# Optimization experiments

Hardware: AMD Instinct MI355X
Metric: run time of the kernel (lower is better)

## Reference

```python
import jax, jax.numpy as jnp
import numpy as np

A, H, HI = 4, 3, 2  # nagents, n_pol_heads, n_intr_rew_heads (sep_extr_head=True)
# leave-one-out index table: row i lists all agents k != i, in ascending order (torch loop order)
LOO = np.array([[k for k in range(A) if k != i] for i in range(A)])  # [A, A-1]


def setup_inputs() -> dict:
    key = jax.random.key(0)
    ks = jax.random.split(key, 12)
    B, S, C, D = 32768, 256, 16, 128  # batch, vect_state_size, action_size, hidden_dim
    IN = C * (A - 1) + D  # 176 critic input dim
    r = lambda k, shp, s=0.05: jax.random.normal(k, shp, dtype=jnp.float32) * s
    return {
        "state_vect": jax.random.normal(ks[0], (B, S), dtype=jnp.float32),
        "acs": jax.random.normal(ks[1], (A, H, B, C), dtype=jnp.float32),
        "enc_W": r(ks[2], (S, D)),
        "enc_b": r(ks[3], (D,)),
        "extr_W1": r(ks[4], (H, A, IN, D)),
        "extr_b1": r(ks[5], (H, A, D)),
        "extr_W2": r(ks[6], (H, A, D, C)),
        "extr_b2": r(ks[7], (H, A, C)),
        "intr_W1": r(ks[8], (HI, A, IN, D)),
        "intr_b1": r(ks[9], (HI, A, D)),
        "intr_W2": r(ks[10], (HI, A, D, C)),
        "intr_b2": r(ks[11], (HI, A, C)),
    }


def reference(state_vect, acs, enc_W, enc_b, extr_W1, extr_b1, extr_W2, extr_b2,
              intr_W1, intr_b1, intr_W2, intr_b2):
    B, C = acs.shape[2], acs.shape[3]
    D = enc_W.shape[1]
    # shared state encoder: Linear -> ReLU
    enc = jax.nn.relu(state_vect @ enc_W + enc_b)  # [B, D]
    # leave-one-out action concat per (agent, head): cat(acs[k!=i, j]) ++ enc
    rel = acs[LOO]                                 # [A, A-1, H, B, C]
    rel = rel.transpose(0, 2, 3, 1, 4).reshape(A, H, B, (A - 1) * C)
    x = jnp.concatenate([rel, jnp.broadcast_to(enc, (A, H, B, D))], axis=-1)  # [A,H,B,IN]
    # greedy action index of agent i's own head-j policy output
    int_acs = jnp.argmax(acs, axis=-1)             # [A, H, B]

    def critic(xin, W1, b1, W2, b2):
        # xin: [A, Hc, B, IN]; W1: [Hc, A, IN, D]; W2: [Hc, A, D, C]
        h = jax.nn.relu(jnp.einsum('ahbi,haid->ahbd', xin, W1)
                        + b1.transpose(1, 0, 2)[:, :, None, :])
        return (jnp.einsum('ahbd,hadc->ahbc', h, W2)
                + b2.transpose(1, 0, 2)[:, :, None, :])  # [A, Hc, B, C]

    extr_all_q = critic(x, extr_W1, extr_b1, extr_W2, extr_b2)          # [A,H,B,C]
    extr_q = jnp.take_along_axis(extr_all_q, int_acs[..., None], axis=-1)  # [A,H,B,1]
    # intr critics exist only for heads j>=1 (sep_extr_head=True -> offset -1)
    intr_all_q = critic(x[:, 1:], intr_W1, intr_b1, intr_W2, intr_b2)   # [A,HI,B,C]
    intr_q = jnp.take_along_axis(intr_all_q, int_acs[:, 1:, :, None], axis=-1)  # [A,HI,B,1]
    return extr_q, intr_q
```

## Files before the change

### kernel.cpp

```cpp
#include <hip/hip_runtime.h>

#define NA 4
#define NH 3
#define NHI 2
#define Bsz 32768
#define Ssz 256
#define Csz 16
#define Dsz 128
#define INsz 176
#define NP 20
#define KP 192
#define GT 2

typedef __bf16 v8bf __attribute__((ext_vector_type(8)));
typedef float v4f __attribute__((ext_vector_type(4)));

#define OFF_ENC    0
#define OFF_ACSBF  8388608
#define OFF_W1F    20971520
#define OFF_ENCWF  21954560
#define OFF_W2T    22020096
#define OFF_AMX    22102016
#define OFF_ZERO   22495232

#define N_ACSROW (NA*NH*Bsz)
#define N_W1F   (NP*192*32)
#define N_ENCWF (256*32)
#define N_W2T   (NP*Csz*Dsz)
#define N_ZERO  16
#define N_PREP  (N_ACSROW+N_W1F+N_ENCWF+N_W2T+N_ZERO)

__global__ __launch_bounds__(256) void prep_kernel(
    const float* __restrict__ acs, const float* __restrict__ encW,
    const float* __restrict__ eW1, const float* __restrict__ iW1,
    const float* __restrict__ eW2, const float* __restrict__ iW2,
    const float* __restrict__ eb1, const float* __restrict__ ib1,
    char* __restrict__ ws)
{
    long tid = (long)blockIdx.x * 256 + threadIdx.x;

    if (tid < N_ACSROW) {
        const float4* src = (const float4*)(acs + (size_t)tid * 16);
        float4 f0 = src[0], f1 = src[1], f2 = src[2], f3 = src[3];
        float v[16] = {f0.x,f0.y,f0.z,f0.w, f1.x,f1.y,f1.z,f1.w,
                       f2.x,f2.y,f2.z,f2.w, f3.x,f3.y,f3.z,f3.w};
        v8bf o0, o1;
        #pragma unroll
        for (int i = 0; i < 8; ++i) { o0[i] = (__bf16)v[i]; o1[i] = (__bf16)v[8 + i]; }
        v8bf* dst = (v8bf*)(ws + OFF_ACSBF) + tid * 2;
        dst[0] = o0; dst[1] = o1;
        float best = v[0]; int bi = 0;
        #pragma unroll
        for (int c = 1; c < 16; ++c) if (v[c] > best) { best = v[c]; bi = c; }
        ((unsigned char*)(ws + OFF_AMX))[tid] = (unsigned char)bi;
        return;
    }
    tid -= N_ACSROW;
    if (tid < N_W1F) {
        const int n4 = (int)(tid & 31) * 4;
        const int k  = (int)((tid >> 5) % 192);
        const int p  = (int)(tid / 6144);
        const float* W1; const float* B1;
        if (p < 12) { int ai = p / 3, hj = p % 3; int wi = hj * NA + ai;
                      W1 = eW1 + (size_t)wi * INsz * Dsz; B1 = eb1 + (size_t)wi * Dsz; }
        else { int qq = p - 12; int ai = qq >> 1, jj = qq & 1; int wi = jj * NA + ai;
               W1 = iW1 + (size_t)wi * INsz * Dsz; B1 = ib1 + (size_t)wi * Dsz; }
        float4 f;
        if (k < INsz)       f = *(const float4*)(W1 + (size_t)k * Dsz + n4);
        else if (k == INsz) f = *(const float4*)(B1 + n4);
        else                f = (float4){0.f, 0.f, 0.f, 0.f};
        const int kc = k >> 5, q = (k >> 3) & 3, j = k & 7;
        __bf16* dst = (__bf16*)(ws + OFF_W1F);
        const float fv[4] = {f.x, f.y, f.z, f.w};
        #pragma unroll
        for (int i = 0; i < 4; ++i) {
            const int n = n4 + i, nt = n >> 4, m = n & 15;
            dst[((size_t)(p * 6 + kc) * 8 + nt) * 512 + (q * 16 + m) * 8 + j] = (__bf16)fv[i];
        }
        return;
    }
    tid -= N_W1F;
    if (tid < N_ENCWF) {
        const int n4 = (int)(tid & 31) * 4;
        const int k  = (int)(tid >> 5);
        float4 f = *(const float4*)(encW + (size_t)k * Dsz + n4);
        const int kc = k >> 5, q = (k >> 3) & 3, j = k & 7;
        __bf16* dst = (__bf16*)(ws + OFF_ENCWF);
        const float fv[4] = {f.x, f.y, f.z, f.w};
        #pragma unroll
        for (int i = 0; i < 4; ++i) {
            const int n = n4 + i, nt = n >> 4, m = n & 15;
            dst[((size_t)kc * 8 + nt) * 512 + (q * 16 + m) * 8 + j] = (__bf16)fv[i];
        }
        return;
    }
    tid -= N_ENCWF;
    if (tid < N_W2T) {
        int d = (int)(tid & 127);
        int rest = (int)(tid >> 7);
        int c = rest & 15, p = rest >> 4;
        const float* W2;
        if (p < 12) { int ai = p / 3, hj = p % 3; W2 = eW2 + (size_t)(hj * NA + ai) * Dsz * Csz; }
        else { int qq = p - 12; int ai = qq >> 1, jj = qq & 1; W2 = iW2 + (size_t)(jj * NA + ai) * Dsz * Csz; }
        const int dlow = d & 15, dt = d >> 4;
        ((__bf16*)(ws + OFF_W2T))[(size_t)p * 2048 + c * 128 + ((dlow ^ c) * 8) + dt]
            = (__bf16)W2[(size_t)d * Csz + c];
        return;
    }
    tid -= N_W2T;
    if (tid < N_ZERO) {
        ((unsigned int*)(ws + OFF_ZERO))[tid] = (tid == 0) ? 0x00003F80u : 0u;
    }
}

__global__ __launch_bounds__(256) void enc_kernel(const float* __restrict__ sv,
                                                  const float* __restrict__ encb,
                                                  char* __restrict__ ws)
{
    __shared__ __bf16 tb[4][16 * 136];

    const int t = threadIdx.x;
    const int wv = t >> 6, lane = t & 63, m = lane & 15, q = lane >> 4;
    const int R = blockIdx.x * 64 + wv * 16 + m;
    const __bf16* encwf = (const __bf16*)(ws + OFF_ENCWF);
    char* enct = ws + OFF_ENC;

    v4f acc[8];
    #pragma unroll
    for (int nt = 0; nt < 8; ++nt) acc[nt] = (v4f){0.f, 0.f, 0.f, 0.f};

    const float* arow = sv + (size_t)R * Ssz + q * 8;
    #pragma unroll
    for (int kc = 0; kc < 8; ++kc) {
        float4 f0 = *(const float4*)(arow + kc * 32);
        float4 f1 = *(const float4*)(arow + kc * 32 + 4);
        v8bf af;
        af[0]=(__bf16)f0.x; af[1]=(__bf16)f0.y; af[2]=(__bf16)f0.z; af[3]=(__bf16)f0.w;
        af[4]=(__bf16)f1.x; af[5]=(__bf16)f1.y; af[6]=(__bf16)f1.z; af[7]=(__bf16)f1.w;
        #pragma unroll
        for (int nt = 0; nt < 8; ++nt) {
            v8bf bf = *(const v8bf*)(encwf + ((size_t)kc * 8 + nt) * 512 + lane * 8);
            acc[nt] = __builtin_amdgcn_mfma_f32_16x16x32_bf16(af, bf, acc[nt], 0, 0, 0);
        }
    }
    #pragma unroll
    for (int nt = 0; nt < 8; ++nt) {
        const float bias = encb[nt * 16 + m];
        #pragma unroll
        for (int rg = 0; rg < 4; ++rg) {
            float v = acc[nt][rg] + bias;
            v = v > 0.f ? v : 0.f;
            tb[wv][(q * 4 + rg) * 136 + nt * 16 + m] = (__bf16)v;
        }
    }
    __syncthreads();
    const int rt = blockIdx.x * 4 + wv;
    #pragma unroll
    for (int kc = 0; kc < 4; ++kc) {
        v8bf v = *(const v8bf*)&tb[wv][m * 136 + kc * 32 + q * 8];
        *(v8bf*)(enct + ((size_t)(rt * 4 + kc) * 64 + lane) * 16) = v;
    }
}

#define LD_AF(D, KC, GG) \
  { _Pragma("unroll") \
    for (int mt_ = 0; mt_ < 4; ++mt_) \
      D[mt_] = *(const v8bf*)(base[KC] + (size_t)((mt_ + 16 * (GG)) * strd[KC])); }

#define MFMA_KC(AF, KC) \
  { _Pragma("unroll") \
    for (int nt_ = 0; nt_ < 8; ++nt_) { \
      v8bf bf_ = *(const v8bf*)&w1s[(size_t)(((KC) * 8 + nt_) * 512) + lane * 8]; \
      acc[0][nt_] = __builtin_amdgcn_mfma_f32_16x16x32_bf16(bf_, AF[0], acc[0][nt_], 0, 0, 0); \
      acc[1][nt_] = __builtin_amdgcn_mfma_f32_16x16x32_bf16(bf_, AF[1], acc[1][nt_], 0, 0, 0); \
      acc[2][nt_] = __builtin_amdgcn_mfma_f32_16x16x32_bf16(bf_, AF[2], acc[2][nt_], 0, 0, 0); \
      acc[3][nt_] = __builtin_amdgcn_mfma_f32_16x16x32_bf16(bf_, AF[3], acc[3][nt_], 0, 0, 0); \
    } }

__global__ __launch_bounds__(256, 2) void critic_kernel(
    const float* __restrict__ eb2, const float* __restrict__ ib2,
    const char* __restrict__ ws, float* __restrict__ out)
{
    __shared__ __bf16 w1s[6 * 8 * 512];
    __shared__ __bf16 w2s[16 * 128];

    const int t = threadIdx.x;
    const int p  = blockIdx.y;
    const int rb = blockIdx.x;
    const int wv = t >> 6, lane = t & 63, m = lane & 15, q = lane >> 4;

    int ai, hj;
    const float* b2;
    float* outp;
    if (p < 12) {
        ai = p / 3; hj = p % 3;
        b2 = eb2 + (size_t)(hj * NA + ai) * Csz;
        outp = out + (size_t)(ai * NH + hj) * Bsz;
    } else {
        const int qq = p - 12; ai = qq >> 1; const int jj = qq & 1; hj = jj + 1;
        b2 = ib2 + (size_t)(jj * NA + ai) * Csz;
        outp = out + (size_t)NA * NH * Bsz + (size_t)(ai * NHI + jj) * Bsz;
    }

    const char* acsb = ws + OFF_ACSBF;
    const char* enct = ws + OFF_ENC;
    const __bf16* w1f = (const __bf16*)(ws + OFF_W1F) + (size_t)p * 6 * 8 * 512;
    const __bf16* w2t = (const __bf16*)(ws + OFF_W2T) + (size_t)p * 2048;
    const unsigned char* amxp = (const unsigned char*)(ws + OFF_AMX)
        + (size_t)(ai * NH + hj) * Bsz + (size_t)rb * 512 + wv * 64;
    const char* zerop = ws + OFF_ZERO;

    {
        const v8bf* src = (const v8bf*)w1f;
        #pragma unroll
        for (int i = 0; i < 12; ++i)
            ((v8bf*)w1s)[i * 256 + t] = src[i * 256 + t];
        ((v8bf*)w2s)[t] = ((const v8bf*)w2t)[t];
    }

    const int loo0 = 0 + (0 >= ai), loo1 = 1 + (1 >= ai), loo2 = 2 + (2 >= ai);
    const size_t rowoff = ((size_t)rb * 512 + wv * 64 + m) * 32;
    const char* pl0 = acsb + (size_t)(loo0 * NH + hj) * Bsz * 32 + rowoff;
    const char* pl1 = acsb + (size_t)(loo1 * NH + hj) * Bsz * 32 + rowoff;
    const char* pl2 = acsb + (size_t)(loo2 * NH + hj) * Bsz * 32 + rowoff;
    const int rt0 = rb * 32 + wv * 4;
    const char* encB = enct + (size_t)rt0 * 4096 + m * 16;

    const char* base[6];
    int strd[6];
    base[0] = (q < 2) ? (pl0 + q * 16) : (pl1 + (q - 2) * 16);           strd[0] = 512;
    base[1] = (q < 2) ? (pl2 + q * 16) : (encB + (q - 2) * 256);         strd[1] = (q < 2) ? 512 : 4096;
    base[2] = encB + (q + 2)  * 256;                                     strd[2] = 4096;
    base[3] = encB + (q + 6)  * 256;                                     strd[3] = 4096;
    base[4] = encB + (q + 10) * 256;                                     strd[4] = 4096;
    base[5] = (q < 2) ? (encB + (14 + q) * 256) : (zerop + (q - 2) * 16);
    strd[5] = (q < 2) ? 4096 : 0;

    v4f acc[4][8];
    #pragma unroll
    for (int i = 0; i < 4; ++i)
        #pragma unroll
        for (int j = 0; j < 8; ++j)
            acc[i][j] = (v4f){0.f, 0.f, 0.f, 0.f};

    v8bf af0[4], af1[4], af2[4];
    LD_AF(af0, 0, 0)
    LD_AF(af1, 1, 0)

    __syncthreads();

    #pragma unroll
    for (int g = 0; g < GT; ++g) {
        int cb[4];
        #pragma unroll
        for (int mt = 0; mt < 4; ++mt)
            cb[mt] = amxp[g * 256 + mt * 16 + m];

        LD_AF(af2, 2, g)  MFMA_KC(af0, 0)
        LD_AF(af0, 3, g)  MFMA_KC(af1, 1)
        LD_AF(af1, 4, g)  MFMA_KC(af2, 2)
        LD_AF(af2, 5, g)  MFMA_KC(af0, 3)
        if (g + 1 < GT) { LD_AF(af0, 0, g + 1) }
        MFMA_KC(af1, 4)
        if (g + 1 < GT) { LD_AF(af1, 1, g + 1) }
        MFMA_KC(af2, 5)

        #pragma unroll
        for (int mt = 0; mt < 4; ++mt) {
            const int c = cb[mt];
            const __bf16* wcb = &w2s[c * 128];
            float s0 = 0.f, s1 = 0.f;
            #pragma unroll
            for (int rg = 0; rg < 4; rg += 2) {
                const v8bf wa = *(const v8bf*)&wcb[((q * 4 + rg) ^ c) * 8];
                const v8bf wb = *(const v8bf*)&wcb[((q * 4 + rg + 1) ^ c) * 8];
                #pragma unroll
                for (int nt = 0; nt < 8; ++nt) {
                    s0 += fmaxf(acc[mt][nt][rg],     0.f) * (float)wa[nt];
                    s1 += fmaxf(acc[mt][nt][rg + 1], 0.f) * (float)wb[nt];
                }
            }
            float tsum = s0 + s1;
            tsum += __shfl_xor(tsum, 16, 64);
            tsum += __shfl_xor(tsum, 32, 64);
            if (q == 0)
                outp[(size_t)rb * 512 + g * 256 + wv * 64 + mt * 16 + m] = tsum + b2[c];
            if (g + 1 < GT) {
                #pragma unroll
                for (int nt = 0; nt < 8; ++nt) acc[mt][nt] = (v4f){0.f, 0.f, 0.f, 0.f};
            }
        }
    }
}

extern "C" void kernel_launch(void* const* d_in, const int* in_sizes, int n_in,
                              void* d_out, int out_size, void* d_ws, size_t ws_size,
                              hipStream_t stream) {
    const float* sv   = (const float*)d_in[0];
    const float* acs  = (const float*)d_in[1];
    const float* encW = (const float*)d_in[2];
    const float* encb = (const float*)d_in[3];
    const float* eW1  = (const float*)d_in[4];
    const float* eb1  = (const float*)d_in[5];
    const float* eW2  = (const float*)d_in[6];
    const float* eb2  = (const float*)d_in[7];
    const float* iW1  = (const float*)d_in[8];
    const float* ib1  = (const float*)d_in[9];
    const float* iW2  = (const float*)d_in[10];
    const float* ib2  = (const float*)d_in[11];
    float* out = (float*)d_out;
    char* ws = (char*)d_ws;

    hipLaunchKernelGGL(prep_kernel, dim3((N_PREP + 255) / 256), dim3(256), 0, stream,
                       acs, encW, eW1, iW1, eW2, iW2, eb1, ib1, ws);
    hipLaunchKernelGGL(enc_kernel, dim3(Bsz / 64), dim3(256), 0, stream, sv, encb, ws);
    hipLaunchKernelGGL(critic_kernel, dim3(Bsz / 512, NP), dim3(256), 0, stream,
                       eb2, ib2, ws, out);
}
```

Before: 162.0 us.

## Reorder K dimension and tile acs bf16 layout for contiguous MFMA fragment loads

Permutes the critic input K ordering so the encoder features come first and the leave-one-out actions last, and rewrites the bf16 action buffer into a row-tile fragment layout. Each wave's A-fragment loads then become contiguous 1KB-per-wave reads with fixed offsets instead of per-lane base/stride tables. It also moves the amax index load after the MFMAs and caches b2 in shared memory. The risk is that the new layouts must match exactly between the prep kernel and the critic kernel.

New measurement: 153.1 us. 1.06x faster.

```diff
diff --git a/kernel.cpp b/kernel.cpp
--- a/kernel.cpp
+++ b/kernel.cpp
@@ -47,8 +47,12 @@
         v8bf o0, o1;
         #pragma unroll
         for (int i = 0; i < 8; ++i) { o0[i] = (__bf16)v[i]; o1[i] = (__bf16)v[8 + i]; }
-        v8bf* dst = (v8bf*)(ws + OFF_ACSBF) + tid * 2;
-        dst[0] = o0; dst[1] = o1;
+        const int plane = (int)(tid >> 15);
+        const int b     = (int)(tid & 32767);
+        const int rt    = b >> 4, mm = b & 15;
+        char* dstb = ws + OFF_ACSBF + (size_t)plane * 1048576 + (size_t)rt * 512 + mm * 16;
+        *(v8bf*)dstb         = o0;
+        *(v8bf*)(dstb + 256) = o1;
         float best = v[0]; int bi = 0;
         #pragma unroll
         for (int c = 1; c < 16; ++c) if (v[c] > best) { best = v[c]; bi = c; }
@@ -66,7 +70,8 @@
         else { int qq = p - 12; int ai = qq >> 1, jj = qq & 1; int wi = jj * NA + ai;
                W1 = iW1 + (size_t)wi * INsz * Dsz; B1 = ib1 + (size_t)wi * Dsz; }
         float4 f;
-        if (k < INsz)       f = *(const float4*)(W1 + (size_t)k * Dsz + n4);
+        if (k < 128)        f = *(const float4*)(W1 + (size_t)(48 + k) * Dsz + n4);
+        else if (k < INsz)  f = *(const float4*)(W1 + (size_t)(k - 128) * Dsz + n4);
         else if (k == INsz) f = *(const float4*)(B1 + n4);
         else                f = (float4){0.f, 0.f, 0.f, 0.f};
         const int kc = k >> 5, q = (k >> 3) & 3, j = k & 7;
@@ -162,10 +167,20 @@
     }
 }
 
-#define LD_AF(D, KC, GG) \
+#define LD_E(D, KC, GG) \
   { _Pragma("unroll") \
     for (int mt_ = 0; mt_ < 4; ++mt_) \
-      D[mt_] = *(const v8bf*)(base[KC] + (size_t)((mt_ + 16 * (GG)) * strd[KC])); }
+      D[mt_] = *(const v8bf*)(encL + (GG) * 65536 + mt_ * 4096 + (KC) * 1024); }
+
+#define LD_4(D, GG) \
+  { _Pragma("unroll") \
+    for (int mt_ = 0; mt_ < 4; ++mt_) \
+      D[mt_] = *(const v8bf*)(a4L + (GG) * 8192 + mt_ * 512); }
+
+#define LD_5(D, GG) \
+  { _Pragma("unroll") \
+    for (int mt_ = 0; mt_ < 4; ++mt_) \
+      D[mt_] = *(const v8bf*)(a5L + (GG) * g5 + mt_ * s5); }
 
 #define MFMA_KC(AF, KC) \
   { _Pragma("unroll") \
@@ -183,6 +198,7 @@
 {
     __shared__ __bf16 w1s[6 * 8 * 512];
     __shared__ __bf16 w2s[16 * 128];
+    __shared__ float  b2s[16];
 
     const int t = threadIdx.x;
     const int p  = blockIdx.y;
@@ -202,13 +218,10 @@
         outp = out + (size_t)NA * NH * Bsz + (size_t)(ai * NHI + jj) * Bsz;
     }
 
-    const char* acsb = ws + OFF_ACSBF;
-    const char* enct = ws + OFF_ENC;
     const __bf16* w1f = (const __bf16*)(ws + OFF_W1F) + (size_t)p * 6 * 8 * 512;
     const __bf16* w2t = (const __bf16*)(ws + OFF_W2T) + (size_t)p * 2048;
     const unsigned char* amxp = (const unsigned char*)(ws + OFF_AMX)
         + (size_t)(ai * NH + hj) * Bsz + (size_t)rb * 512 + wv * 64;
-    const char* zerop = ws + OFF_ZERO;
 
     {
         const v8bf* src = (const v8bf*)w1f;
@@ -216,25 +229,18 @@
         for (int i = 0; i < 12; ++i)
             ((v8bf*)w1s)[i * 256 + t] = src[i * 256 + t];
         ((v8bf*)w2s)[t] = ((const v8bf*)w2t)[t];
+        if (t < 16) b2s[t] = b2[t];
     }
 
     const int loo0 = 0 + (0 >= ai), loo1 = 1 + (1 >= ai), loo2 = 2 + (2 >= ai);
-    const size_t rowoff = ((size_t)rb * 512 + wv * 64 + m) * 32;
-    const char* pl0 = acsb + (size_t)(loo0 * NH + hj) * Bsz * 32 + rowoff;
-    const char* pl1 = acsb + (size_t)(loo1 * NH + hj) * Bsz * 32 + rowoff;
-    const char* pl2 = acsb + (size_t)(loo2 * NH + hj) * Bsz * 32 + rowoff;
-    const int rt0 = rb * 32 + wv * 4;
-    const char* encB = enct + (size_t)rt0 * 4096 + m * 16;
-
-    const char* base[6];
-    int strd[6];
-    base[0] = (q < 2) ? (pl0 + q * 16) : (pl1 + (q - 2) * 16);           strd[0] = 512;
-    base[1] = (q < 2) ? (pl2 + q * 16) : (encB + (q - 2) * 256);         strd[1] = (q < 2) ? 512 : 4096;
-    base[2] = encB + (q + 2)  * 256;                                     strd[2] = 4096;
-    base[3] = encB + (q + 6)  * 256;                                     strd[3] = 4096;
-    base[4] = encB + (q + 10) * 256;                                     strd[4] = 4096;
-    base[5] = (q < 2) ? (encB + (14 + q) * 256) : (zerop + (q - 2) * 16);
-    strd[5] = (q < 2) ? 4096 : 0;
+    const int pA = loo0 * NH + hj, pB = loo1 * NH + hj, pC = loo2 * NH + hj;
+    const int rtb = rb * 32 + wv * 4;
+    const char* encL = ws + OFF_ENC + (size_t)rtb * 4096 + lane * 16;
+    const size_t rtoff = (size_t)rtb * 512 + (lane & 31) * 16;
+    const char* a4L = ws + OFF_ACSBF + (size_t)((q < 2) ? pA : pB) * 1048576 + rtoff;
+    const char* a5L; int s5, g5;
+    if (q < 2) { a5L = ws + OFF_ACSBF + (size_t)pC * 1048576 + rtoff; s5 = 512; g5 = 8192; }
+    else       { a5L = ws + OFF_ZERO + (q - 2) * 16;                  s5 = 0;   g5 = 0;    }
 
     v4f acc[4][8];
     #pragma unroll
@@ -244,26 +250,26 @@
             acc[i][j] = (v4f){0.f, 0.f, 0.f, 0.f};
 
     v8bf af0[4], af1[4], af2[4];
-    LD_AF(af0, 0, 0)
-    LD_AF(af1, 1, 0)
+    LD_E(af0, 0, 0)
+    LD_E(af1, 1, 0)
 
     __syncthreads();
 
     #pragma unroll
     for (int g = 0; g < GT; ++g) {
+        LD_E(af2, 2, g)  MFMA_KC(af0, 0)
+        LD_E(af0, 3, g)  MFMA_KC(af1, 1)
+        LD_4(af1, g)     MFMA_KC(af2, 2)
+        LD_5(af2, g)     MFMA_KC(af0, 3)
+        if (g + 1 < GT) { LD_E(af0, 0, g + 1) }
+        MFMA_KC(af1, 4)
+        if (g + 1 < GT) { LD_E(af1, 1, g + 1) }
+        MFMA_KC(af2, 5)
+
         int cb[4];
         #pragma unroll
         for (int mt = 0; mt < 4; ++mt)
             cb[mt] = amxp[g * 256 + mt * 16 + m];
-
-        LD_AF(af2, 2, g)  MFMA_KC(af0, 0)
-        LD_AF(af0, 3, g)  MFMA_KC(af1, 1)
-        LD_AF(af1, 4, g)  MFMA_KC(af2, 2)
-        LD_AF(af2, 5, g)  MFMA_KC(af0, 3)
-        if (g + 1 < GT) { LD_AF(af0, 0, g + 1) }
-        MFMA_KC(af1, 4)
-        if (g + 1 < GT) { LD_AF(af1, 1, g + 1) }
-        MFMA_KC(af2, 5)
 
         #pragma unroll
         for (int mt = 0; mt < 4; ++mt) {
@@ -284,7 +290,7 @@
             tsum += __shfl_xor(tsum, 16, 64);
             tsum += __shfl_xor(tsum, 32, 64);
             if (q == 0)
-                outp[(size_t)rb * 512 + g * 256 + wv * 64 + mt * 16 + m] = tsum + b2[c];
+                outp[(size_t)rb * 512 + g * 256 + wv * 64 + mt * 16 + m] = tsum + b2s[c];
             if (g + 1 < GT) {
                 #pragma unroll
                 for (int nt = 0; nt < 8; ++nt) acc[mt][nt] = (v4f){0.f, 0.f, 0.f, 0.f};
```
